# Kernel tuning notes

Hardware: AMD Instinct MI355X
Metric: run time of the kernel (lower is better)

## Reference

```python
import jax, jax.numpy as jnp
import numpy as np

EXTENT = 1.0  # kernel-point influence radius (init kwarg 'extent')
B, N, M, H, K, F, C = 4, 16384, 16384, 32, 15, 64, 64


def setup_inputs() -> dict:
    key = jax.random.key(0)
    ks = jax.random.split(key, 6)
    points = jax.random.uniform(ks[0], (B, N, 3), dtype=jnp.float32)
    features = jax.random.normal(ks[1], (B, N, F), dtype=jnp.float32)
    output_points = jax.random.uniform(ks[2], (B, M, 3), dtype=jnp.float32)
    neighbor_indices = jax.random.randint(ks[3], (B, M, H), 0, N)
    # kernel point dispositions inside a ball of radius 1.5*extent (load_kernels stand-in)
    k_points = jax.random.uniform(ks[4], (K, 3), minval=-1.0, maxval=1.0, dtype=jnp.float32) * (1.5 * EXTENT) / jnp.sqrt(3.0)
    k_values = jax.random.normal(ks[5], (K, F, C), dtype=jnp.float32) * 0.05
    return {
        'points': points, 'features': features, 'output_points': output_points,
        'k_points': k_points, 'k_values': k_values, 'neighbor_indices': neighbor_indices,
    }


def reference(points, features, output_points, k_points, k_values, neighbor_indices):
    b, m, h = neighbor_indices.shape
    idx = neighbor_indices.reshape(b, m * h, 1)
    # batched gather (tf.gather batch_dims=1)
    neigh_pts = jnp.take_along_axis(points, idx, axis=1).reshape(b, m, h, 3)
    neigh_feat = jnp.take_along_axis(features, idx, axis=1).reshape(b, m, h, -1)
    # relative coords to each output point, then to each kernel point
    rel = neigh_pts - output_points[:, :, None, :]                # [B,M,H,3]
    diff = rel[:, :, :, None, :] - k_points                       # [B,M,H,K,3]
    sq_d = jnp.sum(diff * diff, axis=-1)                          # [B,M,H,K]
    # linear influence
    w = jnp.maximum(1.0 - jnp.sqrt(sq_d) / EXTENT, 0.0)           # [B,M,H,K]
    # weight neighbor features per kernel point, then apply per-kernel linear map, sum over K
    wf = jnp.einsum('bmhk,bmhf->bmkf', w, neigh_feat)             # [B,M,K,F]
    out = jnp.einsum('bmkf,kfc->bmc', wf, k_values)               # [B,M,C]
    return out
```

## Files before the change

kernel.cpp:

```cpp
#include <hip/hip_runtime.h>

#define BATCH 4
#define NPTS 16384
#define MPTS 16384
#define NH 32
#define NK 15
#define NF 64
#define NC 64

typedef short short8 __attribute__((ext_vector_type(8)));
typedef float floatx4 __attribute__((ext_vector_type(4)));

__device__ __forceinline__ unsigned short f2bf(float x) {
    unsigned int u = __builtin_bit_cast(unsigned int, x);
    u = u + 0x7FFFu + ((u >> 16) & 1u);
    return (unsigned short)(u >> 16);
}

__device__ __forceinline__ unsigned pack_trunc(float lo, float hi) {
    return __builtin_amdgcn_perm(__builtin_bit_cast(unsigned, hi),
                                 __builtin_bit_cast(unsigned, lo), 0x07060302u);
}

__global__ void prep_kernel(const float* __restrict__ kv, const float* __restrict__ feat,
                            unsigned short* __restrict__ vp, unsigned short* __restrict__ featbf) {
    if (blockIdx.x < 32) {
        const int gid = blockIdx.x * 256 + threadIdx.x;
        const int lane = gid & 63;
        const int ct   = (gid >> 6) & 3;
        const int kk   = gid >> 8;
        const int c    = ct * 16 + (lane & 15);
        const int kap0 = kk * 32 + (lane >> 4) * 8;
        unsigned int o[4];
        #pragma unroll
        for (int jj = 0; jj < 4; jj++) {
            unsigned short lo, hi;
            {
                const int kap = kap0 + jj * 2;
                const int f = kap >> 4, k = kap & 15;
                lo = (k < NK) ? f2bf(kv[((size_t)(k * NF + f)) * NC + c]) : (unsigned short)0;
            }
            {
                const int kap = kap0 + jj * 2 + 1;
                const int f = kap >> 4, k = kap & 15;
                hi = (k < NK) ? f2bf(kv[((size_t)(k * NF + f)) * NC + c]) : (unsigned short)0;
            }
            o[jj] = (unsigned)lo | ((unsigned)hi << 16);
        }
        *(uint4*)(vp + (size_t)gid * 8) = make_uint4(o[0], o[1], o[2], o[3]);
    } else {
        const int gid = (blockIdx.x - 32) * 256 + threadIdx.x;
        const size_t base = (size_t)gid * 8;
        float4 a = *(const float4*)(feat + base);
        float4 b = *(const float4*)(feat + base + 4);
        uint4 o;
        o.x = (unsigned)f2bf(a.x) | ((unsigned)f2bf(a.y) << 16);
        o.y = (unsigned)f2bf(a.z) | ((unsigned)f2bf(a.w) << 16);
        o.z = (unsigned)f2bf(b.x) | ((unsigned)f2bf(b.y) << 16);
        o.w = (unsigned)f2bf(b.z) | ((unsigned)f2bf(b.w) << 16);
        *(uint4*)(featbf + base) = o;
    }
}

__global__ __launch_bounds__(256, 5) void kpconv_kernel(
    const float* __restrict__ points,
    const unsigned short* __restrict__ featbf,
    const float* __restrict__ outpts,
    const float* __restrict__ kpts,
    const unsigned short* __restrict__ vp,
    const int*   __restrict__ nbr,
    float* __restrict__ out)
{
    __shared__ __align__(16) unsigned short awf[16 * 512];
    __shared__ __align__(16) unsigned short feat_s[4 * 1160];
    __shared__ int   idx_s[512];
    __shared__ float opt_s[48];
    __shared__ float kp_s[48];

    const int tid   = threadIdx.x;
    const int batch = blockIdx.x & 3;
    const int m0    = (blockIdx.x >> 2) << 4;

    if (tid < 48) kp_s[tid] = (tid < 45) ? kpts[tid] : 1e9f;
    if (tid >= 64 && tid < 112)
        opt_s[tid - 64] = outpts[(size_t)(batch * MPTS + m0) * 3 + (tid - 64)];
    {
        const size_t nb = (size_t)(batch * MPTS + m0) * NH;
        idx_s[tid]       = nbr[nb + tid];
        idx_s[256 + tid] = nbr[nb + 256 + tid];
    }
    __syncthreads();

    const int g    = tid >> 6;
    const int lane = tid & 63;
    const int cl   = lane & 15;
    const int q    = lane >> 4;
    const int sa   = cl;
    const int sfc  = q;

    const unsigned short* fbase = featbf + (size_t)(batch * NPTS) * NF;

    uint4 pra, prb;
    {
        const int srow = g * 32 + sa * 2;
        const int id0 = idx_s[srow], id1 = idx_s[srow + 1];
        pra = *(const uint4*)(fbase + (size_t)id0 * NF + sfc * 8);
        prb = *(const uint4*)(fbase + (size_t)id1 * NF + sfc * 8);
    }

    float4* rel4 = (float4*)awf;
    #pragma unroll
    for (int rr = 0; rr < 2; rr++) {
        const int row = tid * 2 + rr;
        const int id  = idx_s[row];
        const int pm  = row >> 5;
        const float* pp = points + ((size_t)(batch * NPTS) + id) * 3;
        rel4[row] = make_float4(pp[0] - opt_s[pm * 3 + 0],
                                pp[1] - opt_s[pm * 3 + 1],
                                pp[2] - opt_s[pm * 3 + 2], 0.f);
    }
    __syncthreads();

    short8 af[4];
    {
        const float kx = kp_s[cl * 3 + 0];
        const float ky = kp_s[cl * 3 + 1];
        const float kz = kp_s[cl * 3 + 2];
        #pragma unroll
        for (int rp = 0; rp < 4; rp++) {
            const int p = rp * 4 + g;
            float wv[8];
            #pragma unroll
            for (int j = 0; j < 8; j++) {
                const float4 rr = rel4[p * 32 + q * 8 + j];
                const float dx = rr.x - kx, dy = rr.y - ky, dz = rr.z - kz;
                const float d2 = dx * dx + dy * dy + dz * dz;
                wv[j] = fmaxf(1.f - __builtin_amdgcn_sqrtf(d2), 0.f);
            }
            uint4 ua;
            ua.x = pack_trunc(wv[0], wv[1]);
            ua.y = pack_trunc(wv[2], wv[3]);
            ua.z = pack_trunc(wv[4], wv[5]);
            ua.w = pack_trunc(wv[6], wv[7]);
            af[rp] = __builtin_bit_cast(short8, ua);
        }
    }
    __syncthreads();

    floatx4 acc0 = {0.f, 0.f, 0.f, 0.f};
    floatx4 acc1 = {0.f, 0.f, 0.f, 0.f};
    const unsigned short* vpg = vp + g * 512 + lane * 8;
    unsigned short* dp = &feat_s[g * 1160 + sfc * 288 + sa * 2];

    #pragma unroll
    for (int it = 0; it < 8; it++) {
        const int r  = it & 3;
        const int p  = r * 4 + g;

        *(unsigned*)(dp + 0 * 36) = __builtin_amdgcn_perm(prb.x, pra.x, 0x05040100u);
        *(unsigned*)(dp + 1 * 36) = __builtin_amdgcn_perm(prb.x, pra.x, 0x07060302u);
        *(unsigned*)(dp + 2 * 36) = __builtin_amdgcn_perm(prb.y, pra.y, 0x05040100u);
        *(unsigned*)(dp + 3 * 36) = __builtin_amdgcn_perm(prb.y, pra.y, 0x07060302u);
        *(unsigned*)(dp + 4 * 36) = __builtin_amdgcn_perm(prb.z, pra.z, 0x05040100u);
        *(unsigned*)(dp + 5 * 36) = __builtin_amdgcn_perm(prb.z, pra.z, 0x07060302u);
        *(unsigned*)(dp + 6 * 36) = __builtin_amdgcn_perm(prb.w, pra.w, 0x05040100u);
        *(unsigned*)(dp + 7 * 36) = __builtin_amdgcn_perm(prb.w, pra.w, 0x07060302u);

        if (it < 7) {
            const int nit = it + 1;
            const int nfh = nit >> 2, nr = nit & 3;
            const int srow = (nr * 4 + g) * 32 + sa * 2;
            const int id0 = idx_s[srow], id1 = idx_s[srow + 1];
            pra = *(const uint4*)(fbase + (size_t)id0 * NF + nfh * 32 + sfc * 8);
            prb = *(const uint4*)(fbase + (size_t)id1 * NF + nfh * 32 + sfc * 8);
        }

        #pragma unroll
        for (int t = 0; t < 2; t++) {
            const uint4 ub = *(const uint4*)&feat_s[g * 1160 + (t * 16 + cl) * 36 + q * 8];
            floatx4 dd = {0.f, 0.f, 0.f, 0.f};
            dd = __builtin_amdgcn_mfma_f32_16x16x32_bf16(af[r], __builtin_bit_cast(short8, ub), dd, 0, 0, 0);
            const int kk    = 8 * t + (cl >> 1);
            const int q2    = (2 * cl + (q >> 1)) & 3;
            const int chunk = (p ^ kk) | (q2 << 4);
            unsigned* wp = (unsigned*)awf + kk * 256 + chunk * 4 + (q & 1) * 2;
            wp[0] = pack_trunc(dd[0], dd[1]);
            wp[1] = pack_trunc(dd[2], dd[3]);
        }

        if (it == 3) {
            __syncthreads();
            #pragma unroll 4
            for (int kk = 0; kk < 16; kk++) {
                const int chunk = (cl ^ kk) | (lane & 48);
                const uint4 uA = *(const uint4*)&awf[kk * 512 + chunk * 8];
                const uint4 uB = *(const uint4*)(vpg + (size_t)kk * 2048);
                if (kk & 1)
                    acc1 = __builtin_amdgcn_mfma_f32_16x16x32_bf16(
                        __builtin_bit_cast(short8, uA), __builtin_bit_cast(short8, uB), acc1, 0, 0, 0);
                else
                    acc0 = __builtin_amdgcn_mfma_f32_16x16x32_bf16(
                        __builtin_bit_cast(short8, uA), __builtin_bit_cast(short8, uB), acc0, 0, 0, 0);
            }
            __syncthreads();
        }
    }

    __syncthreads();
    #pragma unroll 4
    for (int kk = 0; kk < 16; kk++) {
        const int chunk = (cl ^ kk) | (lane & 48);
        const uint4 uA = *(const uint4*)&awf[kk * 512 + chunk * 8];
        const uint4 uB = *(const uint4*)(vpg + (size_t)(16 + kk) * 2048);
        if (kk & 1)
            acc1 = __builtin_amdgcn_mfma_f32_16x16x32_bf16(
                __builtin_bit_cast(short8, uA), __builtin_bit_cast(short8, uB), acc1, 0, 0, 0);
        else
            acc0 = __builtin_amdgcn_mfma_f32_16x16x32_bf16(
                __builtin_bit_cast(short8, uA), __builtin_bit_cast(short8, uB), acc0, 0, 0, 0);
    }

    __syncthreads();
    float* ob = (float*)awf;
    #pragma unroll
    for (int ri = 0; ri < 4; ri++)
        ob[(q * 4 + ri) * 68 + g * 16 + cl] = acc0[ri] + acc1[ri];
    __syncthreads();
    {
        const int row = tid >> 4;
        const int c4  = tid & 15;
        const floatx4 v = *(const floatx4*)&ob[row * 68 + c4 * 4];
        floatx4* dst = (floatx4*)&out[((size_t)(batch * MPTS + m0 + row)) * NC + c4 * 4];
        __builtin_nontemporal_store(v, dst);
    }
}

extern "C" void kernel_launch(void* const* d_in, const int* in_sizes, int n_in,
                              void* d_out, int out_size, void* d_ws, size_t ws_size,
                              hipStream_t stream) {
    const float* points   = (const float*)d_in[0];
    const float* features = (const float*)d_in[1];
    const float* outpts   = (const float*)d_in[2];
    const float* kpts     = (const float*)d_in[3];
    const float* kvals    = (const float*)d_in[4];
    const int*   nbr      = (const int*)d_in[5];
    float* out = (float*)d_out;

    unsigned short* vp     = (unsigned short*)d_ws;
    unsigned short* featbf = (unsigned short*)((char*)d_ws + 131072);

    prep_kernel<<<2080, 256, 0, stream>>>(kvals, features, vp, featbf);

    const int blocks = BATCH * (MPTS / 16);
    kpconv_kernel<<<blocks, 256, 0, stream>>>(points, featbf, outpts, kpts, vp, nbr, out);
}
```

Baseline: 137.4 us.

## Deepen feature gather prefetch to two stages and pad rel4 LDS layout

Feature gathers from global memory are now double-buffered with a prefetch distance of two iterations instead of one, so each gather has more time to arrive before its data is written to shared memory. Separately, the relative-coordinate array in shared memory gets one float4 of padding after every 8 rows, to reduce bank conflicts when lanes read it during the weight computation. The deeper prefetch holds more registers live, which may lower occupancy, and the padded layout must still fit inside the awf buffer it shares.

```diff
diff --git a/kernel.cpp b/kernel.cpp
--- a/kernel.cpp
+++ b/kernel.cpp
@@ -100,12 +100,16 @@
 
     const unsigned short* fbase = featbf + (size_t)(batch * NPTS) * NF;
 
-    uint4 pra, prb;
-    {
-        const int srow = g * 32 + sa * 2;
-        const int id0 = idx_s[srow], id1 = idx_s[srow + 1];
-        pra = *(const uint4*)(fbase + (size_t)id0 * NF + sfc * 8);
-        prb = *(const uint4*)(fbase + (size_t)id1 * NF + sfc * 8);
+    uint4 praA, prbA, praB, prbB;
+    {
+        const int srow0 = (0 * 4 + g) * 32 + sa * 2;
+        const int ida0 = idx_s[srow0], idb0 = idx_s[srow0 + 1];
+        praA = *(const uint4*)(fbase + (size_t)ida0 * NF + sfc * 8);
+        prbA = *(const uint4*)(fbase + (size_t)idb0 * NF + sfc * 8);
+        const int srow1 = (1 * 4 + g) * 32 + sa * 2;
+        const int ida1 = idx_s[srow1], idb1 = idx_s[srow1 + 1];
+        praB = *(const uint4*)(fbase + (size_t)ida1 * NF + sfc * 8);
+        prbB = *(const uint4*)(fbase + (size_t)idb1 * NF + sfc * 8);
     }
 
     float4* rel4 = (float4*)awf;
@@ -115,9 +119,9 @@
         const int id  = idx_s[row];
         const int pm  = row >> 5;
         const float* pp = points + ((size_t)(batch * NPTS) + id) * 3;
-        rel4[row] = make_float4(pp[0] - opt_s[pm * 3 + 0],
-                                pp[1] - opt_s[pm * 3 + 1],
-                                pp[2] - opt_s[pm * 3 + 2], 0.f);
+        rel4[row + (row >> 3)] = make_float4(pp[0] - opt_s[pm * 3 + 0],
+                                             pp[1] - opt_s[pm * 3 + 1],
+                                             pp[2] - opt_s[pm * 3 + 2], 0.f);
     }
     __syncthreads();
 
@@ -132,7 +136,7 @@
             float wv[8];
             #pragma unroll
             for (int j = 0; j < 8; j++) {
-                const float4 rr = rel4[p * 32 + q * 8 + j];
+                const float4 rr = rel4[36 * p + 9 * q + j];
                 const float dx = rr.x - kx, dy = rr.y - ky, dz = rr.z - kz;
                 const float d2 = dx * dx + dy * dy + dz * dz;
                 wv[j] = fmaxf(1.f - __builtin_amdgcn_sqrtf(d2), 0.f);
@@ -157,22 +161,23 @@
         const int r  = it & 3;
         const int p  = r * 4 + g;
 
-        *(unsigned*)(dp + 0 * 36) = __builtin_amdgcn_perm(prb.x, pra.x, 0x05040100u);
-        *(unsigned*)(dp + 1 * 36) = __builtin_amdgcn_perm(prb.x, pra.x, 0x07060302u);
-        *(unsigned*)(dp + 2 * 36) = __builtin_amdgcn_perm(prb.y, pra.y, 0x05040100u);
-        *(unsigned*)(dp + 3 * 36) = __builtin_amdgcn_perm(prb.y, pra.y, 0x07060302u);
-        *(unsigned*)(dp + 4 * 36) = __builtin_amdgcn_perm(prb.z, pra.z, 0x05040100u);
-        *(unsigned*)(dp + 5 * 36) = __builtin_amdgcn_perm(prb.z, pra.z, 0x07060302u);
-        *(unsigned*)(dp + 6 * 36) = __builtin_amdgcn_perm(prb.w, pra.w, 0x05040100u);
-        *(unsigned*)(dp + 7 * 36) = __builtin_amdgcn_perm(prb.w, pra.w, 0x07060302u);
-
-        if (it < 7) {
-            const int nit = it + 1;
+        *(unsigned*)(dp + 0 * 36) = __builtin_amdgcn_perm(prbA.x, praA.x, 0x05040100u);
+        *(unsigned*)(dp + 1 * 36) = __builtin_amdgcn_perm(prbA.x, praA.x, 0x07060302u);
+        *(unsigned*)(dp + 2 * 36) = __builtin_amdgcn_perm(prbA.y, praA.y, 0x05040100u);
+        *(unsigned*)(dp + 3 * 36) = __builtin_amdgcn_perm(prbA.y, praA.y, 0x07060302u);
+        *(unsigned*)(dp + 4 * 36) = __builtin_amdgcn_perm(prbA.z, praA.z, 0x05040100u);
+        *(unsigned*)(dp + 5 * 36) = __builtin_amdgcn_perm(prbA.z, praA.z, 0x07060302u);
+        *(unsigned*)(dp + 6 * 36) = __builtin_amdgcn_perm(prbA.w, praA.w, 0x05040100u);
+        *(unsigned*)(dp + 7 * 36) = __builtin_amdgcn_perm(prbA.w, praA.w, 0x07060302u);
+
+        praA = praB; prbA = prbB;
+        if (it < 6) {
+            const int nit = it + 2;
             const int nfh = nit >> 2, nr = nit & 3;
             const int srow = (nr * 4 + g) * 32 + sa * 2;
             const int id0 = idx_s[srow], id1 = idx_s[srow + 1];
-            pra = *(const uint4*)(fbase + (size_t)id0 * NF + nfh * 32 + sfc * 8);
-            prb = *(const uint4*)(fbase + (size_t)id1 * NF + nfh * 32 + sfc * 8);
+            praB = *(const uint4*)(fbase + (size_t)id0 * NF + nfh * 32 + sfc * 8);
+            prbB = *(const uint4*)(fbase + (size_t)id1 * NF + nfh * 32 + sfc * 8);
         }
 
         #pragma unroll
```

Measured after the change: 136.7 us. Within noise of the previous version (-0.5%).
